# Performance work log

Hardware: AMD Instinct MI355X
Metric: run time of the kernel (lower is better)

The kernel has to match this reference:

```python
import jax, jax.numpy as jnp
import numpy as np

ALPHA = 16.0
K = 32
NUM_INSTANCES = 8  # samples per class in the batch (required by the original reshape logic)


def setup_inputs() -> dict:
    key = jax.random.key(0)
    n, d = 4096, 128
    inputs = jax.random.normal(key, (n, d), dtype=jnp.float32)
    # identity-sampler style labels: each class appears exactly NUM_INSTANCES times,
    # as assumed by the original pos_dist.resize(...) logic
    targets = (jnp.arange(n) // NUM_INSTANCES).astype(jnp.int64)
    return {"inputs": inputs, "targets": targets}


def reference(inputs, targets):
    n = inputs.shape[0]
    # L2-normalize rows (normalized=True)
    x = inputs / jnp.linalg.norm(inputs, axis=1, keepdims=True)
    # squared euclidean distance matrix: ||xi||^2 + ||xj||^2 - 2 xi.xj
    sq = jnp.sum(x * x, axis=1)  # [n]
    dist = sq[:, None] + sq[None, :] - 2.0 * (x @ x.T)  # [n, n]

    eye = jnp.eye(n, dtype=bool)
    same = targets[:, None] == targets[None, :]
    pos_mask = same & ~eye          # positives, excluding self
    neg_mask = ~same                # negatives

    inf = jnp.float32(jnp.inf)
    # threshold = K-th smallest (0-indexed) among the n-1 off-diagonal dists per row
    row_sorted = jnp.sort(jnp.where(eye, inf, dist), axis=1)
    thr = row_sorted[:, K]  # [n]

    base = jnp.mean(dist, axis=1, keepdims=True)  # mean over full row (incl. diagonal 0)
    below = dist < thr[:, None]
    pos_sel = pos_mask & below
    neg_sel = neg_mask & below

    expo = jnp.exp(ALPHA * (base - dist))  # [n, n]
    pos_logit = jnp.sum(jnp.where(pos_sel, expo, 0.0), axis=1)
    neg_logit = jnp.sum(jnp.where(neg_sel, expo, 0.0), axis=1)

    # fallback when no positive is below the threshold: use the closest positive
    min_pos = jnp.min(jnp.where(pos_mask, dist, inf), axis=1)
    fallback = jnp.exp(ALPHA * (base[:, 0] - min_pos))
    has_pos = jnp.any(pos_sel, axis=1)
    pos_logit = jnp.where(has_pos, pos_logit, fallback)

    loss_i = -jnp.log(pos_logit / (pos_logit + neg_logit))  # [n]
    loss = jnp.mean(loss_i)
    accuracy = jnp.mean((loss_i < 0.6).astype(jnp.float32))
    pos_d = jnp.sum(jnp.where(pos_mask, dist, 0.0)) / jnp.sum(pos_mask)
    neg_d = jnp.sum(jnp.where(neg_mask, dist, 0.0)) / jnp.sum(neg_mask)
    return loss, accuracy, pos_d, neg_d
```

## Files before the change

### kernel.cpp

```cpp
#include <hip/hip_runtime.h>
#include <math.h>

#define N 4096
#define D 128
#define RPB 8
#define NT 512
#define KSEL 32
#define CAND 192
#define ALPHA_C 16.0f

__device__ inline float waveSumF(float v){
  #pragma unroll
  for (int o = 32; o; o >>= 1) v += __shfl_xor(v, o);
  return v;
}
__device__ inline int waveSumI(int v){
  #pragma unroll
  for (int o = 32; o; o >>= 1) v += __shfl_xor(v, o);
  return v;
}
__device__ inline float waveMinF(float v){
  #pragma unroll
  for (int o = 32; o; o >>= 1) v = fminf(v, __shfl_xor(v, o));
  return v;
}
__device__ inline unsigned fkey(float f){
  unsigned u = __float_as_uint(f);
  return u ^ ((u >> 31) ? 0xFFFFFFFFu : 0x80000000u);
}
__device__ inline float fkey_inv(unsigned u){
  unsigned bits = (u & 0x80000000u) ? (u ^ 0x80000000u) : ~u;
  return __uint_as_float(bits);
}

__global__ __launch_bounds__(256) void knorm(const float* __restrict__ in,
                                             float* __restrict__ xn,
                                             float* __restrict__ xnT,
                                             float* __restrict__ sq,
                                             double* __restrict__ accum,
                                             unsigned* __restrict__ ctr){
  if (blockIdx.x == 0 && threadIdx.x < 8){
    if (threadIdx.x < 4) accum[threadIdx.x] = 0.0;
    if (threadIdx.x == 4) *ctr = 0u;
  }
  int row = blockIdx.x * 4 + (threadIdx.x >> 6);
  int lane = threadIdx.x & 63;
  const float* p = in + (size_t)row * D;
  float e0 = p[lane], e1 = p[lane + 64];
  float s = waveSumF(e0*e0 + e1*e1);
  float inv = 1.0f / sqrtf(s);
  float x0 = e0 * inv, x1 = e1 * inv;
  float s2 = waveSumF(x0*x0 + x1*x1);
  xn[(size_t)row * D + lane]      = x0;
  xn[(size_t)row * D + lane + 64] = x1;
  xnT[(size_t)lane * N + row]        = x0;
  xnT[(size_t)(lane + 64) * N + row] = x1;
  if (lane == 0) sq[row] = s2;
}

__global__ __launch_bounds__(NT, 4) void kmain(const float* __restrict__ xn,
                                               const float* __restrict__ xnT,
                                               const float* __restrict__ sq,
                                               const int* __restrict__ tgt,
                                               double* __restrict__ accum,
                                               unsigned* __restrict__ ctr,
                                               float* __restrict__ out){
  __shared__ float xi[RPB][D];
  __shared__ float buf[2][RPB][512];
  __shared__ float cand[RPB][CAND];
  __shared__ int   ccnt[RPB];
  __shared__ float scrB[RPB][RPB];
  __shared__ float scrM[RPB][RPB];
  __shared__ float scrP[RPB], scrN[RPB], lsSh[RPB], acSh[RPB];

  const int tid  = threadIdx.x;
  const int lane = tid & 63;
  const int w    = tid >> 6;
  const int i0   = blockIdx.x * RPB;

  for (int t = tid; t < RPB * D; t += NT)
    (&xi[0][0])[t] = xn[(size_t)i0 * D + t];
  if (lane == 0){
    ccnt[w] = 0;
    #pragma unroll
    for (int t = 0; t < RPB; ++t){ scrB[w][t] = 0.f; scrM[w][t] = INFINITY; }
  }
  __syncthreads();

  const int fA = 128 * w + lane;
  const int fB = fA + 64;
  const float4* T4 = (const float4*)xnT;

  float acc[RPB][8];
  #pragma unroll
  for (int r = 0; r < RPB; ++r)
    #pragma unroll
    for (int q = 0; q < 8; ++q) acc[r][q] = 0.f;

  for (int k = 0; k < D; ++k){
    float4 vA = T4[(size_t)k * (N/4) + fA];
    float4 vB = T4[(size_t)k * (N/4) + fB];
    float xik[RPB];
    #pragma unroll
    for (int r = 0; r < RPB; ++r) xik[r] = xi[r][k];
    #pragma unroll
    for (int r = 0; r < RPB; ++r){
      acc[r][0] += xik[r] * vA.x;  acc[r][1] += xik[r] * vA.y;
      acc[r][2] += xik[r] * vA.z;  acc[r][3] += xik[r] * vA.w;
      acc[r][4] += xik[r] * vB.x;  acc[r][5] += xik[r] * vB.y;
      acc[r][6] += xik[r] * vB.z;  acc[r][7] += xik[r] * vB.w;
    }
  }

  float d[64];
  float posd = 0.f, negd = 0.f;

  #pragma unroll
  for (int rr = 0; rr < 16; ++rr){
    const int h = rr >> 3, t = rr & 7, A = rr & 1;
    const float sqi_t = sq[i0 + t];
    const int   ti_t  = tgt[i0 + t];
    const int f = 128 * w + 64 * h + lane;
    const float4 sq4 = ((const float4*)sq)[f];
    const int4   tg4 = ((const int4*)tgt)[f];
    const int jbase = 4 * f;
    float dv[4]; float pb = 0.f, pm = INFINITY;
    #pragma unroll
    for (int q = 0; q < 4; ++q){
      float sqjq = (q==0)?sq4.x:(q==1)?sq4.y:(q==2)?sq4.z:sq4.w;
      int   tjq  = (q==0)?tg4.x:(q==1)?tg4.y:(q==2)?tg4.z:tg4.w;
      float dj = sqi_t + sqjq - 2.0f * acc[t][h*4 + q];
      pb += dj;
      bool same = (tjq == ti_t);
      bool diag = (jbase + q == i0 + t);
      if (same && !diag){ posd += dj; pm = fminf(pm, dj); }
      if (!same) negd += dj;
      dv[q] = diag ? INFINITY : dj;
    }
    float rb = waveSumF(pb);
    float rm = waveMinF(pm);
    if (lane == 0){ scrB[w][t] += rb; scrM[w][t] = fminf(scrM[w][t], rm); }
    ((float4*)&buf[A][w][4*lane])[0] = make_float4(dv[0], dv[1], dv[2], dv[3]);
    __syncthreads();
    if (w == t){
      #pragma unroll
      for (int wp = 0; wp < 8; ++wp){
        float4 v = ((const float4*)&buf[A][wp][4*lane])[0];
        d[4*(2*wp + h) + 0] = v.x;  d[4*(2*wp + h) + 1] = v.y;
        d[4*(2*wp + h) + 2] = v.z;  d[4*(2*wp + h) + 3] = v.w;
      }
    }
  }

  { float v = waveSumF(posd); if (lane == 0) scrP[w] = v; }
  { float v = waveSumF(negd); if (lane == 0) scrN[w] = v; }
  __syncthreads();

  float base, minpos;
  {
    float bp = (lane < 8) ? scrB[lane][w] : 0.f;
    base = waveSumF(bp) * (1.0f / (float)N);
    float mp = (lane < 8) ? scrM[lane][w] : INFINITY;
    minpos = waveMinF(mp);
  }
  if (tid == 0){
    double sp = 0.0, sn = 0.0;
    #pragma unroll
    for (int r = 0; r < RPB; ++r){ sp += (double)scrP[r]; sn += (double)scrN[r]; }
    atomicAdd(&accum[2], sp);
    atomicAdd(&accum[3], sn);
  }

  float thr;
  {
    float dmin = INFINITY;
    #pragma unroll
    for (int s = 0; s < 64; ++s) dmin = fminf(dmin, d[s]);
    dmin = waveMinF(dmin);

    unsigned lo = fkey(dmin);
    unsigned hi = fkey(4.5f);
    int c = 0; bool have = false; float pvx = 0.f;

    while (hi - lo > 1u){
      float loV = fkey_inv(lo), hiV = fkey_inv(hi);
      unsigned mid = fkey(0.5f * (loV + hiV));
      mid = (mid <= lo) ? lo + 1u : ((mid >= hi) ? hi - 1u : mid);
      float pv = fkey_inv(mid);
      int cc = 0;
      #pragma unroll
      for (int s = 0; s < 64; ++s) cc += (d[s] < pv) ? 1 : 0;
      cc = waveSumI(cc);
      if (cc < KSEL + 1) lo = mid;
      else { hi = mid; if (cc <= CAND){ c = cc; have = true; pvx = pv; break; } }
    }

    if (have){
      #pragma unroll
      for (int s = 0; s < 64; ++s){
        if (d[s] < pvx){
          int ix = atomicAdd(&ccnt[w], 1);
          if (ix < CAND) cand[w][ix] = d[s];
        }
      }
      __threadfence_block();
      #pragma unroll
      for (int m = 0; m < 3; ++m){
        int idx = lane + 64 * m;
        if (idx < c){
          float v = cand[w][idx];
          int rank = 0;
          for (int q2 = 0; q2 < c; ++q2){
            float cq = cand[w][q2];
            rank += (cq < v) || (cq == v && q2 < idx);
          }
          if (rank == KSEL) lsSh[w] = v;
        }
      }
      __threadfence_block();
      thr = lsSh[w];
    } else {
      thr = fkey_inv(lo);
    }
  }

  {
    const int tw = tgt[i0 + w];
    float pls = 0.f, nls = 0.f; int pcnt = 0;
    #pragma unroll
    for (int u = 0; u < 16; ++u){
      int4 tg = ((const int4*)tgt)[64 * u + lane];
      #pragma unroll
      for (int q = 0; q < 4; ++q){
        float dvq = d[4*u + q];
        int   tjq = (q==0)?tg.x:(q==1)?tg.y:(q==2)?tg.z:tg.w;
        if (dvq < thr){
          float e = expf(ALPHA_C * (base - dvq));
          if (tjq == tw){ pls += e; pcnt++; } else nls += e;
        }
      }
    }
    pls = waveSumF(pls); nls = waveSumF(nls); pcnt = waveSumI(pcnt);
    if (lane == 0){
      float plogit = (pcnt > 0) ? pls : expf(ALPHA_C * (base - minpos));
      float li = -logf(plogit / (plogit + nls));
      lsSh[w] = li;
      acSh[w] = (li < 0.6f) ? 1.f : 0.f;
    }
  }
  __syncthreads();
  if (tid == 0){
    float ls = 0.f, ac = 0.f;
    #pragma unroll
    for (int r = 0; r < RPB; ++r){ ls += lsSh[r]; ac += acSh[r]; }
    atomicAdd(&accum[0], (double)ls);
    atomicAdd(&accum[1], (double)ac);
    __threadfence();
    unsigned done = atomicAdd(ctr, 1u);
    if (done == gridDim.x - 1){
      double a0 = atomicAdd(&accum[0], 0.0);
      double a1 = atomicAdd(&accum[1], 0.0);
      double a2 = atomicAdd(&accum[2], 0.0);
      double a3 = atomicAdd(&accum[3], 0.0);
      out[0] = (float)(a0 / (double)N);
      out[1] = (float)(a1 / (double)N);
      out[2] = (float)(a2 / ((double)N * 7.0));
      out[3] = (float)(a3 / ((double)N * (double)(N - 8)));
    }
  }
}

extern "C" void kernel_launch(void* const* d_in, const int* in_sizes, int n_in,
                              void* d_out, int out_size, void* d_ws, size_t ws_size,
                              hipStream_t stream){
  (void)in_sizes; (void)n_in; (void)out_size; (void)ws_size;
  const float* in  = (const float*)d_in[0];
  const int*   tgt = (const int*)d_in[1];
  float* out = (float*)d_out;

  float*    xn    = (float*)d_ws;
  float*    xnT   = xn  + (size_t)N * D;
  float*    sq    = xnT + (size_t)N * D;
  double*   accum = (double*)(sq + N);
  unsigned* ctr   = (unsigned*)(accum + 4);

  knorm <<<N/4, 256, 0, stream>>>(in, xn, xnT, sq, accum, ctr);
  kmain <<<N/RPB, NT, 0, stream>>>(xn, xnT, sq, tgt, accum, ctr, out);
}
```

Baseline: 194.0 us.

## Tile knorm transpose through LDS and split kmain GEMM into halves

The normalization kernel now handles 64 rows per block and stages them in a padded shared tile, so xnT is written with coalesced stores instead of scattered column writes. The main kernel computes the dot products in two halves of 4 columns each rather than 8 at once, which halves the accumulator registers held live alongside d[64]. The launch bound is changed to allow 3 blocks per CU and the exchange buffer is shrunk. Splitting the GEMM means xi is read from shared memory twice as often, and knorm launches far fewer blocks.

```diff
diff --git a/kernel.cpp b/kernel.cpp
--- a/kernel.cpp
+++ b/kernel.cpp
@@ -8,6 +8,7 @@
 #define KSEL 32
 #define CAND 192
 #define ALPHA_C 16.0f
+#define KROWS 64
 
 __device__ inline float waveSumF(float v){
   #pragma unroll
@@ -39,26 +40,37 @@
                                              float* __restrict__ sq,
                                              double* __restrict__ accum,
                                              unsigned* __restrict__ ctr){
-  if (blockIdx.x == 0 && threadIdx.x < 8){
+  __shared__ float tile[KROWS][D + 1];
+  const int w = threadIdx.x >> 6, lane = threadIdx.x & 63;
+  const int r0 = blockIdx.x * KROWS;
+
+  if (blockIdx.x == 0 && threadIdx.x < 5){
     if (threadIdx.x < 4) accum[threadIdx.x] = 0.0;
-    if (threadIdx.x == 4) *ctr = 0u;
-  }
-  int row = blockIdx.x * 4 + (threadIdx.x >> 6);
-  int lane = threadIdx.x & 63;
-  const float* p = in + (size_t)row * D;
-  float e0 = p[lane], e1 = p[lane + 64];
-  float s = waveSumF(e0*e0 + e1*e1);
-  float inv = 1.0f / sqrtf(s);
-  float x0 = e0 * inv, x1 = e1 * inv;
-  float s2 = waveSumF(x0*x0 + x1*x1);
-  xn[(size_t)row * D + lane]      = x0;
-  xn[(size_t)row * D + lane + 64] = x1;
-  xnT[(size_t)lane * N + row]        = x0;
-  xnT[(size_t)(lane + 64) * N + row] = x1;
-  if (lane == 0) sq[row] = s2;
-}
-
-__global__ __launch_bounds__(NT, 4) void kmain(const float* __restrict__ xn,
+    else *ctr = 0u;
+  }
+
+  for (int it = 0; it < 16; ++it){
+    int rl = w * 16 + it;
+    int row = r0 + rl;
+    const float* p = in + (size_t)row * D;
+    float e0 = p[lane], e1 = p[lane + 64];
+    float s = waveSumF(e0*e0 + e1*e1);
+    float inv = 1.0f / sqrtf(s);
+    float x0 = e0 * inv, x1 = e1 * inv;
+    float s2 = waveSumF(x0*x0 + x1*x1);
+    xn[(size_t)row * D + lane]      = x0;
+    xn[(size_t)row * D + lane + 64] = x1;
+    tile[rl][lane] = x0; tile[rl][lane + 64] = x1;
+    if (lane == 0) sq[row] = s2;
+  }
+  __syncthreads();
+  for (int kk = 0; kk < 32; ++kk){
+    int k = 32 * w + kk;
+    xnT[(size_t)k * N + r0 + lane] = tile[lane][k];
+  }
+}
+
+__global__ __launch_bounds__(NT, 3) void kmain(const float* __restrict__ xn,
                                                const float* __restrict__ xnT,
                                                const float* __restrict__ sq,
                                                const int* __restrict__ tgt,
@@ -66,7 +78,7 @@
                                                unsigned* __restrict__ ctr,
                                                float* __restrict__ out){
   __shared__ float xi[RPB][D];
-  __shared__ float buf[2][RPB][512];
+  __shared__ float buf[2][RPB][256];
   __shared__ float cand[RPB][CAND];
   __shared__ int   ccnt[RPB];
   __shared__ float scrB[RPB][RPB];
@@ -87,67 +99,65 @@
   }
   __syncthreads();
 
-  const int fA = 128 * w + lane;
-  const int fB = fA + 64;
   const float4* T4 = (const float4*)xnT;
-
-  float acc[RPB][8];
-  #pragma unroll
-  for (int r = 0; r < RPB; ++r)
-    #pragma unroll
-    for (int q = 0; q < 8; ++q) acc[r][q] = 0.f;
-
-  for (int k = 0; k < D; ++k){
-    float4 vA = T4[(size_t)k * (N/4) + fA];
-    float4 vB = T4[(size_t)k * (N/4) + fB];
-    float xik[RPB];
-    #pragma unroll
-    for (int r = 0; r < RPB; ++r) xik[r] = xi[r][k];
-    #pragma unroll
-    for (int r = 0; r < RPB; ++r){
-      acc[r][0] += xik[r] * vA.x;  acc[r][1] += xik[r] * vA.y;
-      acc[r][2] += xik[r] * vA.z;  acc[r][3] += xik[r] * vA.w;
-      acc[r][4] += xik[r] * vB.x;  acc[r][5] += xik[r] * vB.y;
-      acc[r][6] += xik[r] * vB.z;  acc[r][7] += xik[r] * vB.w;
-    }
-  }
-
   float d[64];
   float posd = 0.f, negd = 0.f;
 
   #pragma unroll
-  for (int rr = 0; rr < 16; ++rr){
-    const int h = rr >> 3, t = rr & 7, A = rr & 1;
-    const float sqi_t = sq[i0 + t];
-    const int   ti_t  = tgt[i0 + t];
+  for (int h = 0; h < 2; ++h){
     const int f = 128 * w + 64 * h + lane;
+    float acc[RPB][4];
+    #pragma unroll
+    for (int r = 0; r < RPB; ++r)
+      #pragma unroll
+      for (int q = 0; q < 4; ++q) acc[r][q] = 0.f;
+
+    for (int k = 0; k < D; ++k){
+      float4 v = T4[(size_t)k * (N/4) + f];
+      float xik[RPB];
+      #pragma unroll
+      for (int r = 0; r < RPB; ++r) xik[r] = xi[r][k];
+      #pragma unroll
+      for (int r = 0; r < RPB; ++r){
+        acc[r][0] += xik[r] * v.x;  acc[r][1] += xik[r] * v.y;
+        acc[r][2] += xik[r] * v.z;  acc[r][3] += xik[r] * v.w;
+      }
+    }
+
     const float4 sq4 = ((const float4*)sq)[f];
     const int4   tg4 = ((const int4*)tgt)[f];
     const int jbase = 4 * f;
-    float dv[4]; float pb = 0.f, pm = INFINITY;
-    #pragma unroll
-    for (int q = 0; q < 4; ++q){
-      float sqjq = (q==0)?sq4.x:(q==1)?sq4.y:(q==2)?sq4.z:sq4.w;
-      int   tjq  = (q==0)?tg4.x:(q==1)?tg4.y:(q==2)?tg4.z:tg4.w;
-      float dj = sqi_t + sqjq - 2.0f * acc[t][h*4 + q];
-      pb += dj;
-      bool same = (tjq == ti_t);
-      bool diag = (jbase + q == i0 + t);
-      if (same && !diag){ posd += dj; pm = fminf(pm, dj); }
-      if (!same) negd += dj;
-      dv[q] = diag ? INFINITY : dj;
-    }
-    float rb = waveSumF(pb);
-    float rm = waveMinF(pm);
-    if (lane == 0){ scrB[w][t] += rb; scrM[w][t] = fminf(scrM[w][t], rm); }
-    ((float4*)&buf[A][w][4*lane])[0] = make_float4(dv[0], dv[1], dv[2], dv[3]);
-    __syncthreads();
-    if (w == t){
-      #pragma unroll
-      for (int wp = 0; wp < 8; ++wp){
-        float4 v = ((const float4*)&buf[A][wp][4*lane])[0];
-        d[4*(2*wp + h) + 0] = v.x;  d[4*(2*wp + h) + 1] = v.y;
-        d[4*(2*wp + h) + 2] = v.z;  d[4*(2*wp + h) + 3] = v.w;
+
+    #pragma unroll
+    for (int t = 0; t < RPB; ++t){
+      const int A = t & 1;
+      const float sqi_t = sq[i0 + t];
+      const int   ti_t  = tgt[i0 + t];
+      float dv[4]; float pb = 0.f, pm = INFINITY;
+      #pragma unroll
+      for (int q = 0; q < 4; ++q){
+        float sqjq = (q==0)?sq4.x:(q==1)?sq4.y:(q==2)?sq4.z:sq4.w;
+        int   tjq  = (q==0)?tg4.x:(q==1)?tg4.y:(q==2)?tg4.z:tg4.w;
+        float dj = sqi_t + sqjq - 2.0f * acc[t][q];
+        pb += dj;
+        bool same = (tjq == ti_t);
+        bool diag = (jbase + q == i0 + t);
+        if (same && !diag){ posd += dj; pm = fminf(pm, dj); }
+        if (!same) negd += dj;
+        dv[q] = diag ? INFINITY : dj;
+      }
+      float rb = waveSumF(pb);
+      float rm = waveMinF(pm);
+      if (lane == 0){ scrB[w][t] += rb; scrM[w][t] = fminf(scrM[w][t], rm); }
+      ((float4*)&buf[A][w][4*lane])[0] = make_float4(dv[0], dv[1], dv[2], dv[3]);
+      __syncthreads();
+      if (w == t){
+        #pragma unroll
+        for (int wp = 0; wp < RPB; ++wp){
+          float4 v = ((const float4*)&buf[A][wp][4*lane])[0];
+          d[4*(2*wp + h) + 0] = v.x;  d[4*(2*wp + h) + 1] = v.y;
+          d[4*(2*wp + h) + 2] = v.z;  d[4*(2*wp + h) + 3] = v.w;
+        }
       }
     }
   }
@@ -284,6 +294,6 @@
   double*   accum = (double*)(sq + N);
   unsigned* ctr   = (unsigned*)(accum + 4);
 
-  knorm <<<N/4, 256, 0, stream>>>(in, xn, xnT, sq, accum, ctr);
+  knorm <<<N/KROWS, 256, 0, stream>>>(in, xn, xnT, sq, accum, ctr);
   kmain <<<N/RPB, NT, 0, stream>>>(xn, xnT, sq, tgt, accum, ctr, out);
 }
```

Result: slower. 242.4 us (+25.0%).
